# Kernel tuning notes

Measured on AMD Instinct MI355X. Metric: run time of the kernel, lower is better.

The kernel has to match this reference:

```python
import jax, jax.numpy as jnp
import numpy as np

DIM = 768
HEADS = 12
HEAD_DIM = 64
INNER = HEADS * HEAD_DIM  # 768


def setup_inputs() -> dict:
    key = jax.random.key(0)
    k_x, k_wqkv, k_bqkv, k_wout, k_bout = jax.random.split(key, 5)
    B, S = 2, 2048
    x = jax.random.normal(k_x, (B, S, DIM), dtype=jnp.float32)
    # nn.Linear(dim, 3*inner): weight [out, in]; store transposed for x @ W
    lim = 1.0 / np.sqrt(DIM)
    w_qkv = jax.random.uniform(k_wqkv, (DIM, 3 * INNER), minval=-lim, maxval=lim, dtype=jnp.float32)
    b_qkv = jax.random.uniform(k_bqkv, (3 * INNER,), minval=-lim, maxval=lim, dtype=jnp.float32)
    lim2 = 1.0 / np.sqrt(INNER)
    # original zero-inits to_out; use random weights so the reference output is non-trivial
    w_out = jax.random.uniform(k_wout, (INNER, DIM), minval=-lim2, maxval=lim2, dtype=jnp.float32)
    b_out = jax.random.uniform(k_bout, (DIM,), minval=-lim2, maxval=lim2, dtype=jnp.float32)
    return {"x": x, "w_qkv": w_qkv, "b_qkv": b_qkv, "w_out": w_out, "b_out": b_out}


def reference(x, w_qkv, b_qkv, w_out, b_out):
    B, S, _ = x.shape
    qkv = x @ w_qkv + b_qkv                               # [B, S, 3*H*D]
    qkv = qkv.reshape(B, S, 3, HEADS, HEAD_DIM)           # b s three h d
    q, k, v = qkv[:, :, 0], qkv[:, :, 1], qkv[:, :, 2]    # each [B, S, H, D]
    scale = 1.0 / np.sqrt(HEAD_DIM)
    # non-causal self-attention (FlashSelfAttention, dropout=0, causal=False)
    scores = jnp.einsum('bshd,bthd->bhst', q, k) * scale  # [B, H, S, S]
    attn = jax.nn.softmax(scores, axis=-1)
    ctx = jnp.einsum('bhst,bthd->bshd', attn, v)          # [B, S, H, D]
    ctx = ctx.reshape(B, S, INNER)
    return ctx @ w_out + b_out                            # [B, S, DIM]
```

## Files before the change

kernel.cpp:

```cpp
#include <hip/hip_runtime.h>
#include <cstddef>
#include <cstdint>

#define DIM  768
#define NH   12
#define HD   64
#define SEQ  2048
#define NB   2
#define NQKV 2304
#define G    (NB * NH * SEQ)

typedef _Float16 f16x8 __attribute__((ext_vector_type(8)));
typedef _Float16 f16x4 __attribute__((ext_vector_type(4)));
typedef __fp16   h16x2 __attribute__((ext_vector_type(2)));
typedef float    f32x4 __attribute__((ext_vector_type(4)));
typedef float    f32x16 __attribute__((ext_vector_type(16)));

#if __has_builtin(__builtin_amdgcn_exp2f)
#define EXP2(x) __builtin_amdgcn_exp2f(x)
#else
#define EXP2(x) exp2f(x)
#endif

#define QSCALE 0.1803368801111244f

__device__ __forceinline__ void gld16(const _Float16* g, _Float16* l) {
  __builtin_amdgcn_global_load_lds(
      (const __attribute__((address_space(1))) void*)g,
      (__attribute__((address_space(3))) void*)l, 16, 0, 0);
}

__device__ __forceinline__ int pkrtz_i(float a, float b) {
  union { h16x2 h; int w; } u;
  u.h = __builtin_amdgcn_cvt_pkrtz(a, b);
  return u.w;
}

__global__ __launch_bounds__(256) void transpose_cvt_kernel(
    const float* __restrict__ W, _Float16* __restrict__ WT, int K, int N) {
  __shared__ _Float16 tl[32][36];
  const int t = threadIdx.x;
  const int k0 = blockIdx.y * 32, n0 = blockIdx.x * 32;
  {
    const int r = t >> 3, c4 = (t & 7) * 4;
    float4 f = *(const float4*)(W + (size_t)(k0 + r) * N + n0 + c4);
    tl[r][c4 + 0] = (_Float16)f.x; tl[r][c4 + 1] = (_Float16)f.y;
    tl[r][c4 + 2] = (_Float16)f.z; tl[r][c4 + 3] = (_Float16)f.w;
  }
  __syncthreads();
  const int n = t >> 3, kc = (t & 7) * 4;
  f16x4 v;
  v[0] = tl[kc + 0][n]; v[1] = tl[kc + 1][n];
  v[2] = tl[kc + 2][n]; v[3] = tl[kc + 3][n];
  *(f16x4*)(WT + (size_t)(n0 + n) * K + k0 + kc) = v;
}

__global__ __launch_bounds__(256) void vtrans_kernel(
    const _Float16* __restrict__ v, _Float16* __restrict__ vT) {
  __shared__ _Float16 tl[64][68];
  const int t = threadIdx.x;
  const int bh = blockIdx.x, st = blockIdx.y;
  const size_t base = (size_t)bh * SEQ * HD;
  {
    const int s = t >> 2, dc = (t & 3) * 16;
    const _Float16* p = v + base + (size_t)(st * 64 + s) * HD + dc;
    f16x8 a = *(const f16x8*)p, b = *(const f16x8*)(p + 8);
    *(f16x8*)&tl[s][dc] = a;
    *(f16x8*)&tl[s][dc + 8] = b;
  }
  __syncthreads();
  const int d = t >> 2, sc = (t & 3) * 16;
  f16x8 o0, o1;
#pragma unroll
  for (int j = 0; j < 8; j++) { o0[j] = tl[sc + j][d]; o1[j] = tl[sc + 8 + j][d]; }
  _Float16* q = vT + base + (size_t)d * SEQ + st * 64 + sc;
  *(f16x8*)q = o0;
  *(f16x8*)(q + 8) = o1;
}

__global__ __launch_bounds__(256) void qkv_gemm_kernel(
    const float* __restrict__ X, const _Float16* __restrict__ BT,
    const float* __restrict__ bias, _Float16* __restrict__ q,
    _Float16* __restrict__ k, _Float16* __restrict__ v) {
  __shared__ _Float16 As[128 * 32];
  __shared__ _Float16 Bs[128 * 32];
  const int tid = threadIdx.x;
  const int lane = tid & 63, wv = tid >> 6;
  const int wm = wv >> 1, wn = wv & 1;
  const int quad = lane >> 4, lcol = lane & 15;
  const int bm = blockIdx.y * 128, bn = blockIdx.x * 128;
  const int K = DIM, N = NQKV;

  f32x4 acc[4][4];
#pragma unroll
  for (int i = 0; i < 4; i++)
#pragma unroll
    for (int j = 0; j < 4; j++) acc[i][j] = (f32x4)(0.f);

  const float* asrc[2];
  _Float16* adst[2];
#pragma unroll
  for (int i = 0; i < 2; i++) {
    const int rA = 64 * i + (tid >> 2);
    const int cc = tid & 3;
    asrc[i] = X + (size_t)(bm + rA) * K + cc * 8;
    adst[i] = As + rA * 32 + ((cc ^ ((rA >> 1) & 3)) * 8);
  }
  const int r0 = wv * 32 + (lane >> 2);
  const int kp = (((lane & 3) ^ ((r0 >> 1) & 3)) * 8);
  const _Float16* b0p = BT + (size_t)(bn + r0) * K + kp;
  const _Float16* b1p = BT + (size_t)(bn + r0 + 16) * K + kp;
  _Float16* lB0 = Bs + (wv * 2 + 0) * 512;
  _Float16* lB1 = Bs + (wv * 2 + 1) * 512;

  for (int k0 = 0; k0 < K; k0 += 32) {
    float4 a0[2], a1[2];
#pragma unroll
    for (int i = 0; i < 2; i++) {
      a0[i] = *(const float4*)(asrc[i] + k0);
      a1[i] = *(const float4*)(asrc[i] + k0 + 4);
    }
    __syncthreads();
    gld16(b0p + k0, lB0);
    gld16(b1p + k0, lB1);
#pragma unroll
    for (int i = 0; i < 2; i++) {
      f16x8 h;
      h[0] = (_Float16)a0[i].x; h[1] = (_Float16)a0[i].y;
      h[2] = (_Float16)a0[i].z; h[3] = (_Float16)a0[i].w;
      h[4] = (_Float16)a1[i].x; h[5] = (_Float16)a1[i].y;
      h[6] = (_Float16)a1[i].z; h[7] = (_Float16)a1[i].w;
      *(f16x8*)adst[i] = h;
    }
    __syncthreads();

    f16x8 af[4], bf[4];
#pragma unroll
    for (int mi = 0; mi < 4; mi++) {
      const int R = wm * 64 + mi * 16 + lcol;
      af[mi] = *(const f16x8*)&As[R * 32 + ((quad ^ ((R >> 1) & 3)) * 8)];
    }
#pragma unroll
    for (int ni = 0; ni < 4; ni++) {
      const int R = wn * 64 + ni * 16 + lcol;
      bf[ni] = *(const f16x8*)&Bs[R * 32 + ((quad ^ ((R >> 1) & 3)) * 8)];
    }
#pragma unroll
    for (int mi = 0; mi < 4; mi++)
#pragma unroll
      for (int ni = 0; ni < 4; ni++)
        acc[mi][ni] = __builtin_amdgcn_mfma_f32_16x16x32_f16(af[mi], bf[ni], acc[mi][ni], 0, 0, 0);
  }

#pragma unroll
  for (int mi = 0; mi < 4; mi++) {
#pragma unroll
    for (int r = 0; r < 4; r++) {
      const int row = bm + wm * 64 + mi * 16 + quad * 4 + r;
      const int b_ = row >> 11, s_ = row & 2047;
#pragma unroll
      for (int ni = 0; ni < 4; ni++) {
        const int c = bn + wn * 64 + ni * 16 + lcol;
        const float val = acc[mi][ni][r] + bias[c];
        const int d = c & 63;
        const int which = c / 768;
        const int h = (c - which * 768) >> 6;
        const size_t idx = (((size_t)b_ * NH + h) * SEQ + s_) * HD + d;
        if (which == 0)      q[idx] = (_Float16)(val * QSCALE);
        else if (which == 1) k[idx] = (_Float16)val;
        else                 v[idx] = (_Float16)val;
      }
    }
  }
}

#define PST 68
#define KSPLIT 4
#define KEYS (SEQ / KSPLIT)
#define TILES (KEYS / 64)
__global__ __launch_bounds__(256, 2) void attn_part_kernel(
    const _Float16* __restrict__ Q, const _Float16* __restrict__ K,
    const _Float16* __restrict__ V, _Float16* __restrict__ Ohat,
    float* __restrict__ L) {
  __shared__ _Float16 Ks[2][64 * PST];
  __shared__ _Float16 Vs[2][64 * PST];
  __shared__ float lsh[4][2][32];
  const int tid = threadIdx.x, lane = tid & 63, wv = tid >> 6;
  const int lr = lane & 31, hw = lane >> 5;
  const int bh = blockIdx.x, qt = blockIdx.y, ks = blockIdx.z;
  const size_t base = (size_t)bh * SEQ * HD;

  f16x8 qb[2][4];
#pragma unroll
  for (int qh = 0; qh < 2; qh++) {
    const _Float16* qp =
        Q + base + (size_t)(qt * 256 + wv * 64 + qh * 32 + lr) * HD + hw * 8;
#pragma unroll
    for (int f = 0; f < 4; f++) qb[qh][f] = *(const f16x8*)(qp + f * 16);
  }

  f32x16 o00 = (f32x16)(0.f), o01 = (f32x16)(0.f);
  f32x16 o10 = (f32x16)(0.f), o11 = (f32x16)(0.f);
  float lpa0 = 0.f, lpb0 = 0.f, lpa1 = 0.f, lpb1 = 0.f;

  const int sr = tid >> 2;
  const int sc = (tid & 3) * 16;
  const _Float16* kp = K + base + (size_t)ks * KEYS * HD + (size_t)sr * HD + sc;
  const _Float16* vp = V + base + ks * KEYS + (size_t)sr * SEQ + sc;

  f16x8 kr0 = *(const f16x8*)kp, kr1 = *(const f16x8*)(kp + 8);
  f16x8 vr0 = *(const f16x8*)vp, vr1 = *(const f16x8*)(vp + 8);
  *(f16x8*)&Ks[0][sr * PST + sc]     = kr0;
  *(f16x8*)&Ks[0][sr * PST + sc + 8] = kr1;
  *(f16x8*)&Vs[0][sr * PST + sc]     = vr0;
  *(f16x8*)&Vs[0][sr * PST + sc + 8] = vr1;
  kr0 = *(const f16x8*)(kp + 64 * HD); kr1 = *(const f16x8*)(kp + 64 * HD + 8);
  vr0 = *(const f16x8*)(vp + 64);      vr1 = *(const f16x8*)(vp + 64 + 8);
  asm volatile("s_waitcnt lgkmcnt(0)" ::: "memory");

  for (int t = 0; t < TILES; t++) {
    const int cur = t & 1;
    __builtin_amdgcn_s_barrier();
    __builtin_amdgcn_sched_barrier(0);

    f16x8 ka0[4], ka1[4];
#pragma unroll
    for (int f = 0; f < 4; f++) {
      ka0[f] = *(const f16x8*)&Ks[cur][lr * PST + f * 16 + hw * 8];
      ka1[f] = *(const f16x8*)&Ks[cur][(32 + lr) * PST + f * 16 + hw * 8];
    }

    f32x16 s00 = (f32x16)(0.f), s01 = (f32x16)(0.f);
    f32x16 s10 = (f32x16)(0.f), s11 = (f32x16)(0.f);
    __builtin_amdgcn_s_setprio(1);
#pragma unroll
    for (int f = 0; f < 4; f++) {
      s00 = __builtin_amdgcn_mfma_f32_32x32x16_f16(ka0[f], qb[0][f], s00, 0, 0, 0);
      s01 = __builtin_amdgcn_mfma_f32_32x32x16_f16(ka1[f], qb[0][f], s01, 0, 0, 0);
      s10 = __builtin_amdgcn_mfma_f32_32x32x16_f16(ka0[f], qb[1][f], s10, 0, 0, 0);
      s11 = __builtin_amdgcn_mfma_f32_32x32x16_f16(ka1[f], qb[1][f], s11, 0, 0, 0);
    }
    __builtin_amdgcn_s_setprio(0);

    f16x8 pf0[4], pf1[4];
#pragma unroll
    for (int f = 0; f < 4; f++) {
      const f32x16& sv = (f < 2) ? s00 : s01;
      const int r0 = (f & 1) * 8;
      const float e0 = EXP2(sv[r0 + 0]), e1 = EXP2(sv[r0 + 1]);
      const float e2 = EXP2(sv[r0 + 2]), e3 = EXP2(sv[r0 + 3]);
      const float e4 = EXP2(sv[r0 + 4]), e5 = EXP2(sv[r0 + 5]);
      const float e6 = EXP2(sv[r0 + 6]), e7 = EXP2(sv[r0 + 7]);
      lpa0 += (e0 + e1) + (e2 + e3);
      lpb0 += (e4 + e5) + (e6 + e7);
      const int a01 = pkrtz_i(e0, e1), b45 = pkrtz_i(e4, e5);
      const int c23 = pkrtz_i(e2, e3), d67 = pkrtz_i(e6, e7);
      auto w02 = __builtin_amdgcn_permlane32_swap(a01, b45, false, false);
      auto w13 = __builtin_amdgcn_permlane32_swap(c23, d67, false, false);
      union { f16x8 h; int w[4]; } pu;
      pu.w[0] = w02[0]; pu.w[1] = w13[0]; pu.w[2] = w02[1]; pu.w[3] = w13[1];
      pf0[f] = pu.h;
    }
#pragma unroll
    for (int f = 0; f < 4; f++) {
      const f32x16& sv = (f < 2) ? s10 : s11;
      const int r0 = (f & 1) * 8;
      const float e0 = EXP2(sv[r0 + 0]), e1 = EXP2(sv[r0 + 1]);
      const float e2 = EXP2(sv[r0 + 2]), e3 = EXP2(sv[r0 + 3]);
      const float e4 = EXP2(sv[r0 + 4]), e5 = EXP2(sv[r0 + 5]);
      const float e6 = EXP2(sv[r0 + 6]), e7 = EXP2(sv[r0 + 7]);
      lpa1 += (e0 + e1) + (e2 + e3);
      lpb1 += (e4 + e5) + (e6 + e7);
      const int a01 = pkrtz_i(e0, e1), b45 = pkrtz_i(e4, e5);
      const int c23 = pkrtz_i(e2, e3), d67 = pkrtz_i(e6, e7);
      auto w02 = __builtin_amdgcn_permlane32_swap(a01, b45, false, false);
      auto w13 = __builtin_amdgcn_permlane32_swap(c23, d67, false, false);
      union { f16x8 h; int w[4]; } pu;
      pu.w[0] = w02[0]; pu.w[1] = w13[0]; pu.w[2] = w02[1]; pu.w[3] = w13[1];
      pf1[f] = pu.h;
    }

    __builtin_amdgcn_s_setprio(1);
#pragma unroll
    for (int f = 0; f < 4; f++) {
      f16x8 vb0 = *(const f16x8*)&Vs[cur][lr * PST + f * 16 + hw * 8];
      f16x8 vb1 = *(const f16x8*)&Vs[cur][(32 + lr) * PST + f * 16 + hw * 8];
      o00 = __builtin_amdgcn_mfma_f32_32x32x16_f16(pf0[f], vb0, o00, 0, 0, 0);
      o01 = __builtin_amdgcn_mfma_f32_32x32x16_f16(pf0[f], vb1, o01, 0, 0, 0);
      o10 = __builtin_amdgcn_mfma_f32_32x32x16_f16(pf1[f], vb0, o10, 0, 0, 0);
      o11 = __builtin_amdgcn_mfma_f32_32x32x16_f16(pf1[f], vb1, o11, 0, 0, 0);
    }
    __builtin_amdgcn_s_setprio(0);

    if (t + 1 < TILES) {
      const int nxt = cur ^ 1;
      *(f16x8*)&Ks[nxt][sr * PST + sc]     = kr0;
      *(f16x8*)&Ks[nxt][sr * PST + sc + 8] = kr1;
      *(f16x8*)&Vs[nxt][sr * PST + sc]     = vr0;
      *(f16x8*)&Vs[nxt][sr * PST + sc + 8] = vr1;
      if (t + 2 < TILES) {
        const _Float16* kn = kp + (size_t)(t + 2) * 64 * HD;
        const _Float16* vn = vp + (t + 2) * 64;
        kr0 = *(const f16x8*)kn; kr1 = *(const f16x8*)(kn + 8);
        vr0 = *(const f16x8*)vn; vr1 = *(const f16x8*)(vn + 8);
      }
      asm volatile("s_waitcnt lgkmcnt(0)" ::: "memory");
    }
  }

  float l0 = lpa0 + lpb0; l0 += __shfl_xor(l0, 32);
  float l1 = lpa1 + lpb1; l1 += __shfl_xor(l1, 32);
  __syncthreads();
  if (hw == 0) { lsh[wv][0][lr] = l0; lsh[wv][1][lr] = l1; }
  __syncthreads();

#pragma unroll
  for (int qh = 0; qh < 2; qh++) {
    const f32x16& oa = qh ? o10 : o00;
    const f32x16& ob = qh ? o11 : o01;
    const size_t rbase =
        (size_t)ks * G + (size_t)bh * SEQ + qt * 256 + wv * 64 + qh * 32;
    if (hw == 0) L[rbase + lr] = qh ? l1 : l0;
    float linv[16];
#pragma unroll
    for (int r = 0; r < 16; r++)
      linv[r] = 1.00048828125f / lsh[wv][qh][(r & 3) + 8 * (r >> 2) + 4 * hw];
#pragma unroll
    for (int r = 0; r < 16; r++) {
      const int rr = (r & 3) + 8 * (r >> 2) + 4 * hw;
      _Float16* cp = Ohat + (rbase + rr) * HD;
      cp[lr]      = (_Float16)(oa[r] * linv[r]);
      cp[32 + lr] = (_Float16)(ob[r] * linv[r]);
    }
  }
}

__global__ __launch_bounds__(256) void out_gemm_kernel(
    const _Float16* __restrict__ Ohat, const float* __restrict__ L,
    const _Float16* __restrict__ WT, const float* __restrict__ bias,
    float* __restrict__ out) {
  __shared__ _Float16 As[64 * 36];
  __shared__ _Float16 Bs[64 * 36];
  const int tid = threadIdx.x, lane = tid & 63, wv = tid >> 6;
  const int wr = (wv >> 1) * 32, wc = (wv & 1) * 32;
  const int quad = lane >> 4, lcol = lane & 15;
  const int bm = blockIdx.y * 64, bn = blockIdx.x * 64;

  f32x4 acc[2][2];
#pragma unroll
  for (int i = 0; i < 2; i++)
#pragma unroll
    for (int j = 0; j < 2; j++) acc[i][j] = (f32x4)(0.f);

  const int ra = tid >> 2, ca = (tid & 3) * 8;
  const int grow = bm + ra, b_ = grow >> 11, s_ = grow & 2047;

  for (int k0 = 0; k0 < DIM; k0 += 32) {
    const int h = k0 >> 6;
    const int lidx = (b_ * NH + h) * SEQ + s_;
    const size_t obase = (size_t)lidx * HD + (k0 & 32) + ca;
    f16x8 u0 = *(const f16x8*)(Ohat + obase);
    f16x8 u1 = *(const f16x8*)(Ohat + (size_t)G * HD + obase);
    f16x8 u2 = *(const f16x8*)(Ohat + 2 * (size_t)G * HD + obase);
    f16x8 u3 = *(const f16x8*)(Ohat + 3 * (size_t)G * HD + obase);
    const float l0 = L[lidx], l1 = L[G + lidx];
    const float l2 = L[2 * G + lidx], l3 = L[3 * G + lidx];
    const float inv = 1.0f / ((l0 + l1) + (l2 + l3));
    const float w0 = l0 * inv, w1 = l1 * inv, w2 = l2 * inv, w3 = l3 * inv;
    f16x8 bv = *(const f16x8*)(WT + (size_t)(bn + ra) * DIM + k0 + ca);

    __syncthreads();
    f16x8 av;
#pragma unroll
    for (int j = 0; j < 8; j++)
      av[j] = (_Float16)((w0 * (float)u0[j] + w1 * (float)u1[j]) +
                         (w2 * (float)u2[j] + w3 * (float)u3[j]));
    *(f16x8*)&As[ra * 36 + ca] = av;
    *(f16x8*)&Bs[ra * 36 + ca] = bv;
    __syncthreads();

    f16x8 af[2], bf[2];
#pragma unroll
    for (int mi = 0; mi < 2; mi++)
      af[mi] = *(const f16x8*)&As[(wr + mi * 16 + lcol) * 36 + quad * 8];
#pragma unroll
    for (int ni = 0; ni < 2; ni++)
      bf[ni] = *(const f16x8*)&Bs[(wc + ni * 16 + lcol) * 36 + quad * 8];
#pragma unroll
    for (int mi = 0; mi < 2; mi++)
#pragma unroll
      for (int ni = 0; ni < 2; ni++)
        acc[mi][ni] = __builtin_amdgcn_mfma_f32_16x16x32_f16(af[mi], bf[ni], acc[mi][ni], 0, 0, 0);
  }

#pragma unroll
  for (int mi = 0; mi < 2; mi++) {
#pragma unroll
    for (int r = 0; r < 4; r++) {
      const int row = bm + wr + mi * 16 + quad * 4 + r;
#pragma unroll
      for (int ni = 0; ni < 2; ni++) {
        const int col = bn + wc + ni * 16 + lcol;
        out[(size_t)row * DIM + col] = acc[mi][ni][r] + bias[col];
      }
    }
  }
}

extern "C" void kernel_launch(void* const* d_in, const int* in_sizes, int n_in,
                              void* d_out, int out_size, void* d_ws,
                              size_t ws_size, hipStream_t stream) {
  const float* x = (const float*)d_in[0];
  const float* w_qkv = (const float*)d_in[1];
  const float* b_qkv = (const float*)d_in[2];
  const float* w_out = (const float*)d_in[3];
  const float* b_out = (const float*)d_in[4];
  float* out = (float*)d_out;

  _Float16* wsh = (_Float16*)d_ws;
  size_t off = 0;
  const size_t hsz = (size_t)NB * NH * SEQ * HD;
  _Float16* wqkvT = wsh + off; off += (size_t)NQKV * DIM;
  _Float16* woutT = wsh + off; off += (size_t)DIM * DIM;
  _Float16* qh   = wsh + off; off += hsz;
  _Float16* kh   = wsh + off; off += hsz;
  _Float16* vh   = wsh + off; off += hsz;
  _Float16* vT   = wsh + off; off += hsz;
  _Float16* Ohat = wsh + off; off += 4 * hsz;
  float*    Lbuf = (float*)(wsh + off);

  transpose_cvt_kernel<<<dim3(NQKV / 32, DIM / 32), 256, 0, stream>>>(w_qkv, wqkvT, DIM, NQKV);
  transpose_cvt_kernel<<<dim3(DIM / 32, DIM / 32), 256, 0, stream>>>(w_out, woutT, DIM, DIM);
  qkv_gemm_kernel<<<dim3(NQKV / 128, (NB * SEQ) / 128), 256, 0, stream>>>(
      x, wqkvT, b_qkv, qh, kh, vh);
  vtrans_kernel<<<dim3(NB * NH, SEQ / 64), 256, 0, stream>>>(vh, vT);
  attn_part_kernel<<<dim3(NB * NH, SEQ / 256, KSPLIT), 256, 0, stream>>>(
      qh, kh, vT, Ohat, Lbuf);
  out_gemm_kernel<<<dim3(DIM / 64, (NB * SEQ) / 64), 256, 0, stream>>>(
      Ohat, Lbuf, woutT, b_out, out);
}
```

Before: 182.2 us.

## Fuse V transpose into QKV GEMM epilogue and halve attention key split

The QKV GEMM epilogue now writes V directly in transposed layout: each V tile is staged through an enlarged shared buffer and then stored as vectors, so the separate vtrans kernel and the intermediate V buffer go away. The attention key split drops from four partitions to two, which halves the partial-output buffer and simplifies the merge in the output GEMM. The trade is half as many attention blocks, so less parallelism and a longer serial key loop per block, plus more shared memory in the QKV GEMM that may lower its occupancy.

Result: no change. 183.1 us (+0.5%).

```diff
diff --git a/kernel.cpp b/kernel.cpp
--- a/kernel.cpp
+++ b/kernel.cpp
@@ -55,41 +55,19 @@
   *(f16x4*)(WT + (size_t)(n0 + n) * K + k0 + kc) = v;
 }
 
-__global__ __launch_bounds__(256) void vtrans_kernel(
-    const _Float16* __restrict__ v, _Float16* __restrict__ vT) {
-  __shared__ _Float16 tl[64][68];
-  const int t = threadIdx.x;
-  const int bh = blockIdx.x, st = blockIdx.y;
-  const size_t base = (size_t)bh * SEQ * HD;
-  {
-    const int s = t >> 2, dc = (t & 3) * 16;
-    const _Float16* p = v + base + (size_t)(st * 64 + s) * HD + dc;
-    f16x8 a = *(const f16x8*)p, b = *(const f16x8*)(p + 8);
-    *(f16x8*)&tl[s][dc] = a;
-    *(f16x8*)&tl[s][dc + 8] = b;
-  }
-  __syncthreads();
-  const int d = t >> 2, sc = (t & 3) * 16;
-  f16x8 o0, o1;
-#pragma unroll
-  for (int j = 0; j < 8; j++) { o0[j] = tl[sc + j][d]; o1[j] = tl[sc + 8 + j][d]; }
-  _Float16* q = vT + base + (size_t)d * SEQ + st * 64 + sc;
-  *(f16x8*)q = o0;
-  *(f16x8*)(q + 8) = o1;
-}
-
 __global__ __launch_bounds__(256) void qkv_gemm_kernel(
     const float* __restrict__ X, const _Float16* __restrict__ BT,
     const float* __restrict__ bias, _Float16* __restrict__ q,
-    _Float16* __restrict__ k, _Float16* __restrict__ v) {
-  __shared__ _Float16 As[128 * 32];
-  __shared__ _Float16 Bs[128 * 32];
+    _Float16* __restrict__ k, _Float16* __restrict__ vT) {
+  __shared__ _Float16 smem[128 * 136];
+  _Float16* As = smem;
+  _Float16* Bs = smem + 128 * 32;
   const int tid = threadIdx.x;
   const int lane = tid & 63, wv = tid >> 6;
   const int wm = wv >> 1, wn = wv & 1;
   const int quad = lane >> 4, lcol = lane & 15;
   const int bm = blockIdx.y * 128, bn = blockIdx.x * 128;
-  const int K = DIM, N = NQKV;
+  const int K = DIM;
 
   f32x4 acc[4][4];
 #pragma unroll
@@ -152,30 +130,61 @@
         acc[mi][ni] = __builtin_amdgcn_mfma_f32_16x16x32_f16(af[mi], bf[ni], acc[mi][ni], 0, 0, 0);
   }
 
-#pragma unroll
-  for (int mi = 0; mi < 4; mi++) {
-#pragma unroll
-    for (int r = 0; r < 4; r++) {
-      const int row = bm + wm * 64 + mi * 16 + quad * 4 + r;
-      const int b_ = row >> 11, s_ = row & 2047;
-#pragma unroll
-      for (int ni = 0; ni < 4; ni++) {
-        const int c = bn + wn * 64 + ni * 16 + lcol;
-        const float val = acc[mi][ni][r] + bias[c];
-        const int d = c & 63;
-        const int which = c / 768;
-        const int h = (c - which * 768) >> 6;
-        const size_t idx = (((size_t)b_ * NH + h) * SEQ + s_) * HD + d;
-        if (which == 0)      q[idx] = (_Float16)(val * QSCALE);
-        else if (which == 1) k[idx] = (_Float16)val;
-        else                 v[idx] = (_Float16)val;
+  const int which = bn / 768;
+  if (which < 2) {
+#pragma unroll
+    for (int mi = 0; mi < 4; mi++) {
+#pragma unroll
+      for (int r = 0; r < 4; r++) {
+        const int row = bm + wm * 64 + mi * 16 + quad * 4 + r;
+        const int b_ = row >> 11, s_ = row & 2047;
+#pragma unroll
+        for (int ni = 0; ni < 4; ni++) {
+          const int c = bn + wn * 64 + ni * 16 + lcol;
+          const float val = acc[mi][ni][r] + bias[c];
+          const int d = c & 63;
+          const int h = (c - which * 768) >> 6;
+          const size_t idx = (((size_t)b_ * NH + h) * SEQ + s_) * HD + d;
+          if (which == 0) q[idx] = (_Float16)(val * QSCALE);
+          else            k[idx] = (_Float16)val;
+        }
       }
     }
+  } else {
+    __syncthreads();
+    _Float16* vtile = smem;
+#pragma unroll
+    for (int mi = 0; mi < 4; mi++) {
+#pragma unroll
+      for (int r = 0; r < 4; r++) {
+        const int sl = wm * 64 + mi * 16 + quad * 4 + r;
+#pragma unroll
+        for (int ni = 0; ni < 4; ni++) {
+          const int dl = wn * 64 + ni * 16 + lcol;
+          const float val = acc[mi][ni][r] + bias[bn + dl];
+          vtile[dl * 136 + sl] = (_Float16)val;
+        }
+      }
+    }
+    __syncthreads();
+    const int b_ = bm >> 11, s0 = bm & 2047;
+    const int h0 = (bn - 1536) >> 6;
+#pragma unroll
+    for (int g = 0; g < 4; g++) {
+      const int dl = g * 32 + (tid >> 3);
+      const int h = h0 + (dl >> 6), d = dl & 63;
+      _Float16* dst = vT + (((size_t)b_ * NH + h) * HD + d) * SEQ + s0;
+#pragma unroll
+      for (int h2 = 0; h2 < 2; h2++) {
+        const int sc = (tid & 7) * 8 + h2 * 64;
+        *(f16x8*)(dst + sc) = *(const f16x8*)&vtile[dl * 136 + sc];
+      }
+    }
   }
 }
 
 #define PST 68
-#define KSPLIT 4
+#define KSPLIT 2
 #define KEYS (SEQ / KSPLIT)
 #define TILES (KEYS / 64)
 __global__ __launch_bounds__(256, 2) void attn_part_kernel(
@@ -192,11 +201,11 @@
 
   f16x8 qb[2][4];
 #pragma unroll
-  for (int qh = 0; qh < 2; qh++) {
+  for (int qs = 0; qs < 2; qs++) {
     const _Float16* qp =
-        Q + base + (size_t)(qt * 256 + wv * 64 + qh * 32 + lr) * HD + hw * 8;
-#pragma unroll
-    for (int f = 0; f < 4; f++) qb[qh][f] = *(const f16x8*)(qp + f * 16);
+        Q + base + (size_t)(qt * 256 + wv * 64 + qs * 32 + lr) * HD + hw * 8;
+#pragma unroll
+    for (int f = 0; f < 4; f++) qb[qs][f] = *(const f16x8*)(qp + f * 16);
   }
 
   f32x16 o00 = (f32x16)(0.f), o01 = (f32x16)(0.f);
@@ -315,16 +324,16 @@
   __syncthreads();
 
 #pragma unroll
-  for (int qh = 0; qh < 2; qh++) {
-    const f32x16& oa = qh ? o10 : o00;
-    const f32x16& ob = qh ? o11 : o01;
+  for (int qs = 0; qs < 2; qs++) {
+    const f32x16& oa = qs ? o10 : o00;
+    const f32x16& ob = qs ? o11 : o01;
     const size_t rbase =
-        (size_t)ks * G + (size_t)bh * SEQ + qt * 256 + wv * 64 + qh * 32;
-    if (hw == 0) L[rbase + lr] = qh ? l1 : l0;
+        (size_t)ks * G + (size_t)bh * SEQ + qt * 256 + wv * 64 + qs * 32;
+    if (hw == 0) L[rbase + lr] = qs ? l1 : l0;
     float linv[16];
 #pragma unroll
     for (int r = 0; r < 16; r++)
-      linv[r] = 1.00048828125f / lsh[wv][qh][(r & 3) + 8 * (r >> 2) + 4 * hw];
+      linv[r] = 1.00048828125f / lsh[wv][qs][(r & 3) + 8 * (r >> 2) + 4 * hw];
 #pragma unroll
     for (int r = 0; r < 16; r++) {
       const int rr = (r & 3) + 8 * (r >> 2) + 4 * hw;
@@ -361,20 +370,15 @@
     const size_t obase = (size_t)lidx * HD + (k0 & 32) + ca;
     f16x8 u0 = *(const f16x8*)(Ohat + obase);
     f16x8 u1 = *(const f16x8*)(Ohat + (size_t)G * HD + obase);
-    f16x8 u2 = *(const f16x8*)(Ohat + 2 * (size_t)G * HD + obase);
-    f16x8 u3 = *(const f16x8*)(Ohat + 3 * (size_t)G * HD + obase);
     const float l0 = L[lidx], l1 = L[G + lidx];
-    const float l2 = L[2 * G + lidx], l3 = L[3 * G + lidx];
-    const float inv = 1.0f / ((l0 + l1) + (l2 + l3));
-    const float w0 = l0 * inv, w1 = l1 * inv, w2 = l2 * inv, w3 = l3 * inv;
+    const float w0 = l0 / (l0 + l1), w1 = 1.0f - w0;
     f16x8 bv = *(const f16x8*)(WT + (size_t)(bn + ra) * DIM + k0 + ca);
 
     __syncthreads();
     f16x8 av;
 #pragma unroll
     for (int j = 0; j < 8; j++)
-      av[j] = (_Float16)((w0 * (float)u0[j] + w1 * (float)u1[j]) +
-                         (w2 * (float)u2[j] + w3 * (float)u3[j]));
+      av[j] = (_Float16)(w0 * (float)u0[j] + w1 * (float)u1[j]);
     *(f16x8*)&As[ra * 36 + ca] = av;
     *(f16x8*)&Bs[ra * 36 + ca] = bv;
     __syncthreads();
@@ -424,16 +428,14 @@
   _Float16* woutT = wsh + off; off += (size_t)DIM * DIM;
   _Float16* qh   = wsh + off; off += hsz;
   _Float16* kh   = wsh + off; off += hsz;
-  _Float16* vh   = wsh + off; off += hsz;
   _Float16* vT   = wsh + off; off += hsz;
-  _Float16* Ohat = wsh + off; off += 4 * hsz;
+  _Float16* Ohat = wsh + off; off += 2 * hsz;
   float*    Lbuf = (float*)(wsh + off);
 
   transpose_cvt_kernel<<<dim3(NQKV / 32, DIM / 32), 256, 0, stream>>>(w_qkv, wqkvT, DIM, NQKV);
   transpose_cvt_kernel<<<dim3(DIM / 32, DIM / 32), 256, 0, stream>>>(w_out, woutT, DIM, DIM);
   qkv_gemm_kernel<<<dim3(NQKV / 128, (NB * SEQ) / 128), 256, 0, stream>>>(
-      x, wqkvT, b_qkv, qh, kh, vh);
-  vtrans_kernel<<<dim3(NB * NH, SEQ / 64), 256, 0, stream>>>(vh, vT);
+      x, wqkvT, b_qkv, qh, kh, vT);
   attn_part_kernel<<<dim3(NB * NH, SEQ / 256, KSPLIT), 256, 0, stream>>>(
       qh, kh, vT, Ohat, Lbuf);
   out_gemm_kernel<<<dim3(DIM / 64, (NB * SEQ) / 64), 256, 0, stream>>>(
```

## Double-buffer QKV GEMM with register prefetch and halve attention key split

Applied to the files above, without the earlier changes.

The QKV GEMM gets double-buffered LDS tiles with register prefetch of the next K-slab. The async global_load_lds path is replaced by ordinary loads, and there is one barrier per step plus priority hints around the MFMAs, so global latency overlaps compute. Attention KSPLIT drops from 4 to 2. That halves the partial-output buffers and simplifies the combine in the output GEMM, but it gives the attention kernel half as many blocks, each doing twice the key tiles.

Measured after the change: 170.7 us. -6.3%, faster.

```diff
diff --git a/kernel.cpp b/kernel.cpp
--- a/kernel.cpp
+++ b/kernel.cpp
@@ -23,12 +23,6 @@
 #endif
 
 #define QSCALE 0.1803368801111244f
-
-__device__ __forceinline__ void gld16(const _Float16* g, _Float16* l) {
-  __builtin_amdgcn_global_load_lds(
-      (const __attribute__((address_space(1))) void*)g,
-      (__attribute__((address_space(3))) void*)l, 16, 0, 0);
-}
 
 __device__ __forceinline__ int pkrtz_i(float a, float b) {
   union { h16x2 h; int w; } u;
@@ -78,18 +72,19 @@
   *(f16x8*)(q + 8) = o1;
 }
 
-__global__ __launch_bounds__(256) void qkv_gemm_kernel(
+#define QKV_STEPS (DIM / 32)
+__global__ __launch_bounds__(256, 2) void qkv_gemm_kernel(
     const float* __restrict__ X, const _Float16* __restrict__ BT,
     const float* __restrict__ bias, _Float16* __restrict__ q,
     _Float16* __restrict__ k, _Float16* __restrict__ v) {
-  __shared__ _Float16 As[128 * 32];
-  __shared__ _Float16 Bs[128 * 32];
+  __shared__ _Float16 As[2][128 * 32];
+  __shared__ _Float16 Bs[2][128 * 32];
   const int tid = threadIdx.x;
   const int lane = tid & 63, wv = tid >> 6;
   const int wm = wv >> 1, wn = wv & 1;
   const int quad = lane >> 4, lcol = lane & 15;
   const int bm = blockIdx.y * 128, bn = blockIdx.x * 128;
-  const int K = DIM, N = NQKV;
+  const int K = DIM;
 
   f32x4 acc[4][4];
 #pragma unroll
@@ -98,58 +93,99 @@
     for (int j = 0; j < 4; j++) acc[i][j] = (f32x4)(0.f);
 
   const float* asrc[2];
-  _Float16* adst[2];
+  int aoff[2];
 #pragma unroll
   for (int i = 0; i < 2; i++) {
     const int rA = 64 * i + (tid >> 2);
     const int cc = tid & 3;
     asrc[i] = X + (size_t)(bm + rA) * K + cc * 8;
-    adst[i] = As + rA * 32 + ((cc ^ ((rA >> 1) & 3)) * 8);
+    aoff[i] = rA * 32 + ((cc ^ ((rA >> 1) & 3)) * 8);
   }
   const int r0 = wv * 32 + (lane >> 2);
-  const int kp = (((lane & 3) ^ ((r0 >> 1) & 3)) * 8);
-  const _Float16* b0p = BT + (size_t)(bn + r0) * K + kp;
-  const _Float16* b1p = BT + (size_t)(bn + r0 + 16) * K + kp;
-  _Float16* lB0 = Bs + (wv * 2 + 0) * 512;
-  _Float16* lB1 = Bs + (wv * 2 + 1) * 512;
-
-  for (int k0 = 0; k0 < K; k0 += 32) {
-    float4 a0[2], a1[2];
-#pragma unroll
-    for (int i = 0; i < 2; i++) {
-      a0[i] = *(const float4*)(asrc[i] + k0);
-      a1[i] = *(const float4*)(asrc[i] + k0 + 4);
-    }
-    __syncthreads();
-    gld16(b0p + k0, lB0);
-    gld16(b1p + k0, lB1);
-#pragma unroll
-    for (int i = 0; i < 2; i++) {
-      f16x8 h;
-      h[0] = (_Float16)a0[i].x; h[1] = (_Float16)a0[i].y;
-      h[2] = (_Float16)a0[i].z; h[3] = (_Float16)a0[i].w;
-      h[4] = (_Float16)a1[i].x; h[5] = (_Float16)a1[i].y;
-      h[6] = (_Float16)a1[i].z; h[7] = (_Float16)a1[i].w;
-      *(f16x8*)adst[i] = h;
-    }
-    __syncthreads();
+  const int kpos = (((lane & 3) ^ ((r0 >> 1) & 3)) * 8);
+  const _Float16* b0p = BT + (size_t)(bn + r0) * K + kpos;
+  const _Float16* b1p = BT + (size_t)(bn + r0 + 16) * K + kpos;
+  const int boff0 = r0 * 32 + (lane & 3) * 8;
+  const int boff1 = (r0 + 16) * 32 + (lane & 3) * 8;
+
+  float4 a0[2], a1[2];
+  f16x8 br0, br1;
+#pragma unroll
+  for (int i = 0; i < 2; i++) {
+    a0[i] = *(const float4*)(asrc[i]);
+    a1[i] = *(const float4*)(asrc[i] + 4);
+  }
+  br0 = *(const f16x8*)b0p;
+  br1 = *(const f16x8*)b1p;
+#pragma unroll
+  for (int i = 0; i < 2; i++) {
+    f16x8 h;
+    h[0] = (_Float16)a0[i].x; h[1] = (_Float16)a0[i].y;
+    h[2] = (_Float16)a0[i].z; h[3] = (_Float16)a0[i].w;
+    h[4] = (_Float16)a1[i].x; h[5] = (_Float16)a1[i].y;
+    h[6] = (_Float16)a1[i].z; h[7] = (_Float16)a1[i].w;
+    *(f16x8*)&As[0][aoff[i]] = h;
+  }
+  *(f16x8*)&Bs[0][boff0] = br0;
+  *(f16x8*)&Bs[0][boff1] = br1;
+#pragma unroll
+  for (int i = 0; i < 2; i++) {
+    a0[i] = *(const float4*)(asrc[i] + 32);
+    a1[i] = *(const float4*)(asrc[i] + 32 + 4);
+  }
+  br0 = *(const f16x8*)(b0p + 32);
+  br1 = *(const f16x8*)(b1p + 32);
+  asm volatile("s_waitcnt lgkmcnt(0)" ::: "memory");
+
+  for (int t = 0; t < QKV_STEPS; t++) {
+    const int cur = t & 1;
+    __builtin_amdgcn_s_barrier();
+    __builtin_amdgcn_sched_barrier(0);
 
     f16x8 af[4], bf[4];
 #pragma unroll
     for (int mi = 0; mi < 4; mi++) {
       const int R = wm * 64 + mi * 16 + lcol;
-      af[mi] = *(const f16x8*)&As[R * 32 + ((quad ^ ((R >> 1) & 3)) * 8)];
+      af[mi] = *(const f16x8*)&As[cur][R * 32 + ((quad ^ ((R >> 1) & 3)) * 8)];
     }
 #pragma unroll
     for (int ni = 0; ni < 4; ni++) {
       const int R = wn * 64 + ni * 16 + lcol;
-      bf[ni] = *(const f16x8*)&Bs[R * 32 + ((quad ^ ((R >> 1) & 3)) * 8)];
-    }
+      bf[ni] = *(const f16x8*)&Bs[cur][R * 32 + ((quad ^ ((R >> 1) & 3)) * 8)];
+    }
+    __builtin_amdgcn_s_setprio(1);
 #pragma unroll
     for (int mi = 0; mi < 4; mi++)
 #pragma unroll
       for (int ni = 0; ni < 4; ni++)
         acc[mi][ni] = __builtin_amdgcn_mfma_f32_16x16x32_f16(af[mi], bf[ni], acc[mi][ni], 0, 0, 0);
+    __builtin_amdgcn_s_setprio(0);
+
+    if (t + 1 < QKV_STEPS) {
+      const int nxt = cur ^ 1;
+#pragma unroll
+      for (int i = 0; i < 2; i++) {
+        f16x8 h;
+        h[0] = (_Float16)a0[i].x; h[1] = (_Float16)a0[i].y;
+        h[2] = (_Float16)a0[i].z; h[3] = (_Float16)a0[i].w;
+        h[4] = (_Float16)a1[i].x; h[5] = (_Float16)a1[i].y;
+        h[6] = (_Float16)a1[i].z; h[7] = (_Float16)a1[i].w;
+        *(f16x8*)&As[nxt][aoff[i]] = h;
+      }
+      *(f16x8*)&Bs[nxt][boff0] = br0;
+      *(f16x8*)&Bs[nxt][boff1] = br1;
+      if (t + 2 < QKV_STEPS) {
+        const int k2 = (t + 2) * 32;
+#pragma unroll
+        for (int i = 0; i < 2; i++) {
+          a0[i] = *(const float4*)(asrc[i] + k2);
+          a1[i] = *(const float4*)(asrc[i] + k2 + 4);
+        }
+        br0 = *(const f16x8*)(b0p + k2);
+        br1 = *(const f16x8*)(b1p + k2);
+      }
+      asm volatile("s_waitcnt lgkmcnt(0)" ::: "memory");
+    }
   }
 
 #pragma unroll
@@ -175,7 +211,7 @@
 }
 
 #define PST 68
-#define KSPLIT 4
+#define KSPLIT 2
 #define KEYS (SEQ / KSPLIT)
 #define TILES (KEYS / 64)
 __global__ __launch_bounds__(256, 2) void attn_part_kernel(
@@ -192,11 +228,11 @@
 
   f16x8 qb[2][4];
 #pragma unroll
-  for (int qh = 0; qh < 2; qh++) {
+  for (int qs = 0; qs < 2; qs++) {
     const _Float16* qp =
-        Q + base + (size_t)(qt * 256 + wv * 64 + qh * 32 + lr) * HD + hw * 8;
-#pragma unroll
-    for (int f = 0; f < 4; f++) qb[qh][f] = *(const f16x8*)(qp + f * 16);
+        Q + base + (size_t)(qt * 256 + wv * 64 + qs * 32 + lr) * HD + hw * 8;
+#pragma unroll
+    for (int f = 0; f < 4; f++) qb[qs][f] = *(const f16x8*)(qp + f * 16);
   }
 
   f32x16 o00 = (f32x16)(0.f), o01 = (f32x16)(0.f);
@@ -315,16 +351,16 @@
   __syncthreads();
 
 #pragma unroll
-  for (int qh = 0; qh < 2; qh++) {
-    const f32x16& oa = qh ? o10 : o00;
-    const f32x16& ob = qh ? o11 : o01;
+  for (int qs = 0; qs < 2; qs++) {
+    const f32x16& oa = qs ? o10 : o00;
+    const f32x16& ob = qs ? o11 : o01;
     const size_t rbase =
-        (size_t)ks * G + (size_t)bh * SEQ + qt * 256 + wv * 64 + qh * 32;
-    if (hw == 0) L[rbase + lr] = qh ? l1 : l0;
+        (size_t)ks * G + (size_t)bh * SEQ + qt * 256 + wv * 64 + qs * 32;
+    if (hw == 0) L[rbase + lr] = qs ? l1 : l0;
     float linv[16];
 #pragma unroll
     for (int r = 0; r < 16; r++)
-      linv[r] = 1.00048828125f / lsh[wv][qh][(r & 3) + 8 * (r >> 2) + 4 * hw];
+      linv[r] = 1.00048828125f / lsh[wv][qs][(r & 3) + 8 * (r >> 2) + 4 * hw];
 #pragma unroll
     for (int r = 0; r < 16; r++) {
       const int rr = (r & 3) + 8 * (r >> 2) + 4 * hw;
@@ -361,20 +397,15 @@
     const size_t obase = (size_t)lidx * HD + (k0 & 32) + ca;
     f16x8 u0 = *(const f16x8*)(Ohat + obase);
     f16x8 u1 = *(const f16x8*)(Ohat + (size_t)G * HD + obase);
-    f16x8 u2 = *(const f16x8*)(Ohat + 2 * (size_t)G * HD + obase);
-    f16x8 u3 = *(const f16x8*)(Ohat + 3 * (size_t)G * HD + obase);
     const float l0 = L[lidx], l1 = L[G + lidx];
-    const float l2 = L[2 * G + lidx], l3 = L[3 * G + lidx];
-    const float inv = 1.0f / ((l0 + l1) + (l2 + l3));
-    const float w0 = l0 * inv, w1 = l1 * inv, w2 = l2 * inv, w3 = l3 * inv;
+    const float w0 = l0 / (l0 + l1), w1 = 1.0f - w0;
     f16x8 bv = *(const f16x8*)(WT + (size_t)(bn + ra) * DIM + k0 + ca);
 
     __syncthreads();
     f16x8 av;
 #pragma unroll
     for (int j = 0; j < 8; j++)
-      av[j] = (_Float16)((w0 * (float)u0[j] + w1 * (float)u1[j]) +
-                         (w2 * (float)u2[j] + w3 * (float)u3[j]));
+      av[j] = (_Float16)(w0 * (float)u0[j] + w1 * (float)u1[j]);
     *(f16x8*)&As[ra * 36 + ca] = av;
     *(f16x8*)&Bs[ra * 36 + ca] = bv;
     __syncthreads();
@@ -426,7 +457,7 @@
   _Float16* kh   = wsh + off; off += hsz;
   _Float16* vh   = wsh + off; off += hsz;
   _Float16* vT   = wsh + off; off += hsz;
-  _Float16* Ohat = wsh + off; off += 4 * hsz;
+  _Float16* Ohat = wsh + off; off += 2 * hsz;
   float*    Lbuf = (float*)(wsh + off);
 
   transpose_cvt_kernel<<<dim3(NQKV / 32, DIM / 32), 256, 0, stream>>>(w_qkv, wqkvT, DIM, NQKV);
```
